# Performance work log

Hardware: AMD Instinct MI355X
Metric: run time of the kernel (lower is better)

The kernel has to match this reference:

```python
import jax, jax.numpy as jnp
import numpy as np

H = 2880      # hidden_size
NH = 64       # num query heads
NKV = 8       # num kv heads
D = 64        # head_dim
G = NH // NKV # GQA group size
W = 128       # sliding window (keys per query, incl. self)
THETA = 150000.0
N = 1024      # tokens


def setup_inputs() -> dict:
    key = jax.random.key(0)
    k0, k1, k2, k3 = jax.random.split(key, 4)
    hidden_states = jax.random.normal(k0, (N, H), jnp.float32)
    Wqkv = jax.random.normal(k1, (H, (NH + 2 * NKV) * D), jnp.float32) * (H ** -0.5)
    Wo = jax.random.normal(k2, (NH * D, H), jnp.float32) * ((NH * D) ** -0.5)
    sinks = jax.random.normal(k3, (NH,), jnp.float32)
    positions = jnp.arange(N, dtype=jnp.int64)
    return {"hidden_states": hidden_states, "Wqkv": Wqkv, "Wo": Wo,
            "sinks": sinks, "positions": positions}


def _rope(x, pos):
    # NeoX-style rotary over full head_dim. x: [n, h, D], pos: [n]
    half = D // 2
    inv_freq = 1.0 / (THETA ** (jnp.arange(half, dtype=jnp.float32) / half))
    ang = pos[:, None].astype(jnp.float32) * inv_freq          # [n, half]
    cos = jnp.cos(ang)[:, None, :]
    sin = jnp.sin(ang)[:, None, :]
    x1, x2 = x[..., :half], x[..., half:]
    return jnp.concatenate([x1 * cos - x2 * sin, x2 * cos + x1 * sin], axis=-1)


def reference(hidden_states, Wqkv, Wo, sinks, positions):
    n = hidden_states.shape[0]
    qkv = hidden_states @ Wqkv
    q, k, v = jnp.split(qkv, [NH * D, NH * D + NKV * D], axis=-1)
    q = _rope(q.reshape(n, NH, D), positions)   # [n, NH, D]
    k = _rope(k.reshape(n, NKV, D), positions)  # [n, NKV, D]
    v = v.reshape(n, NKV, D)

    # Sliding-window key indices: query i attends keys j in [i-W+1, i]
    idx = positions[:, None] - (W - 1) + jnp.arange(W)[None, :]  # [n, W]
    valid = idx >= 0
    idx = jnp.clip(idx, 0, n - 1)
    k_win = k[idx]  # [n, W, NKV, D]
    v_win = v[idx]  # [n, W, NKV, D]

    qg = q.reshape(n, NKV, G, D)
    scores = jnp.einsum('nkgd,nwkd->nkgw', qg, k_win) * (D ** -0.5)
    scores = jnp.where(valid[:, None, None, :], scores, -jnp.inf)

    # Attention sinks: softmax over [scores, sink_logit]; sink gets no value.
    sink = sinks.reshape(NKV, G)                      # [NKV, G]
    m = jnp.maximum(scores.max(-1), sink[None])       # [n, NKV, G]
    p = jnp.exp(scores - m[..., None])                # [n, NKV, G, W]
    denom = p.sum(-1) + jnp.exp(sink[None] - m)       # [n, NKV, G]
    out = jnp.einsum('nkgw,nwkd->nkgd', p, v_win) / denom[..., None]
    return out.reshape(n, NH * D) @ Wo
```

## Files before the change

kernel.cpp:

```cpp
#include <hip/hip_runtime.h>
#include <hip/hip_bf16.h>

#define HDIM   2880
#define NH     64
#define NKV    8
#define DHEAD  64
#define GQ     (NH / NKV)
#define WIN    128
#define NTOK   1024
#define QKV_N  ((NH + 2 * NKV) * DHEAD)
#define QCOLS  (NH * DHEAD)
#define KOFF   QCOLS
#define VOFF   (QCOLS + NKV * DHEAD)

typedef __attribute__((ext_vector_type(8))) short short8;
typedef __attribute__((ext_vector_type(4))) float floatx4;

__device__ unsigned short g_Xb   [(size_t)NTOK  * HDIM];
__device__ unsigned short g_qkvb [(size_t)NTOK  * QKV_N];
__device__ unsigned short g_attn [(size_t)NTOK  * QCOLS];
__device__ unsigned short g_WqkvT[(size_t)QKV_N * HDIM];
__device__ unsigned short g_WoT  [(size_t)HDIM * QCOLS];

__device__ __forceinline__ unsigned short f2b(float f) {
    __hip_bfloat16 h = __float2bfloat16(f);
    return *reinterpret_cast<unsigned short*>(&h);
}

__device__ __forceinline__ void gload_lds16(const unsigned short* g, unsigned short* l) {
    __builtin_amdgcn_global_load_lds(
        (const __attribute__((address_space(1))) unsigned int*)g,
        (__attribute__((address_space(3))) unsigned int*)l, 16, 0, 0);
}

__device__ __forceinline__ void transpose_tile(
        const float* __restrict__ in, unsigned short* __restrict__ out,
        int K, int N, int bk, int bn, int t, unsigned short* T) {
    #pragma unroll
    for (int i = 0; i < 4; ++i) {
        int c = i * 256 + t;
        int r = c >> 4, cc = (c & 15) * 4;
        float4 v = *(const float4*)(in + (size_t)(bk * 64 + r) * N + bn * 64 + cc);
        int col = (((cc >> 2) ^ ((r >> 3) & 7)) << 2);
        T[r * 72 + col + 0] = f2b(v.x);
        T[r * 72 + col + 1] = f2b(v.y);
        T[r * 72 + col + 2] = f2b(v.z);
        T[r * 72 + col + 3] = f2b(v.w);
    }
    __syncthreads();
    #pragma unroll
    for (int i = 0; i < 2; ++i) {
        int c = i * 256 + t;
        int rn = c >> 3, kc = (c & 7) * 8;
        int s = (kc >> 3) & 7;
        int col = ((((rn >> 2) ^ s) << 2) | (rn & 3));
        int4 vv;
        unsigned short* tp = (unsigned short*)&vv;
        #pragma unroll
        for (int j = 0; j < 8; ++j) tp[j] = T[(kc + j) * 72 + col];
        *(int4*)(out + (size_t)(bn * 64 + rn) * K + bk * 64 + kc) = vv;
    }
}

#define NB_WQKV (45 * 80)
#define NB_WO   (64 * 45)
#define NB_CVT  (NTOK * HDIM / 4 / 256)
__global__ __launch_bounds__(256) void prep(
        const float* __restrict__ X, const float* __restrict__ Wqkv,
        const float* __restrict__ Wo, unsigned short* __restrict__ Xb,
        unsigned short* __restrict__ WqkvT, unsigned short* __restrict__ WoT) {
    __shared__ __align__(16) unsigned short T[64 * 72];
    int id = blockIdx.x;
    int t = threadIdx.x;
    if (id < NB_WQKV) {
        transpose_tile(Wqkv, WqkvT, HDIM, QKV_N, id % 45, id / 45, t, T);
    } else if (id < NB_WQKV + NB_WO) {
        int id2 = id - NB_WQKV;
        transpose_tile(Wo, WoT, QCOLS, HDIM, id2 % 64, id2 / 64, t, T);
    } else {
        int gid = (id - NB_WQKV - NB_WO) * 256 + t;
        float4 v = *(const float4*)(X + (size_t)gid * 4);
        ushort4 o;
        o.x = f2b(v.x); o.y = f2b(v.y); o.z = f2b(v.z); o.w = f2b(v.w);
        *(ushort4*)(Xb + (size_t)gid * 4) = o;
    }
}

template<int KLEN, int MODE, int NBN>
__global__ __launch_bounds__(256) void gemm_dir(
        const unsigned short* __restrict__ A, const unsigned short* __restrict__ Bt,
        void* __restrict__ outp) {
    int d0 = blockIdx.x;
    int work = (d0 & 7) * NBN + (d0 >> 3);
    int bm = work & 7, bn = work >> 3;
    int t = threadIdx.x, lane = t & 63, wid = t >> 6;
    int quad = lane >> 4, ml = lane & 15;
    __shared__ __align__(16) unsigned short As[2][128 * 64];
    __shared__ __align__(16) unsigned short Bs[2][64 * 64];
    floatx4 acc[2][4];
    #pragma unroll
    for (int i = 0; i < 2; ++i)
        #pragma unroll
        for (int j = 0; j < 4; ++j) acc[i][j] = (floatx4){0.f, 0.f, 0.f, 0.f};

    int srow = lane >> 3;
    int scol = ((lane & 7) ^ srow) * 8;
    const unsigned short* Ab = A  + (size_t)(bm * 128) * KLEN;
    const unsigned short* Bb = Bt + (size_t)(bn * 64) * KLEN;

    constexpr int NT = KLEN / 64;

    #pragma unroll
    for (int j = 0; j < 4; ++j) {
        int grp = wid * 4 + j;
        int r = grp * 8 + srow;
        gload_lds16(Ab + (size_t)r * KLEN + scol, &As[0][grp * 512]);
    }
    #pragma unroll
    for (int j = 0; j < 2; ++j) {
        int grp = wid * 2 + j;
        int r = grp * 8 + srow;
        gload_lds16(Bb + (size_t)r * KLEN + scol, &Bs[0][grp * 512]);
    }
    __syncthreads();

    for (int ti = 0; ti < NT; ++ti) {
        int cur = ti & 1;
        if (ti + 1 < NT) {
            int k0 = (ti + 1) * 64;
            int nxt = cur ^ 1;
            #pragma unroll
            for (int j = 0; j < 4; ++j) {
                int grp = wid * 4 + j;
                int r = grp * 8 + srow;
                gload_lds16(Ab + (size_t)r * KLEN + k0 + scol, &As[nxt][grp * 512]);
            }
            #pragma unroll
            for (int j = 0; j < 2; ++j) {
                int grp = wid * 2 + j;
                int r = grp * 8 + srow;
                gload_lds16(Bb + (size_t)r * KLEN + k0 + scol, &Bs[nxt][grp * 512]);
            }
        }
        #pragma unroll
        for (int kk = 0; kk < 64; kk += 32) {
            const int ub = kk >> 3;
            int usw = ((ub + quad) ^ (ml & 7)) * 8;
            short8 af[2], bf[4];
            #pragma unroll
            for (int mt = 0; mt < 2; ++mt)
                af[mt] = *(const short8*)&As[cur][(wid * 32 + mt * 16 + ml) * 64 + usw];
            #pragma unroll
            for (int nt = 0; nt < 4; ++nt)
                bf[nt] = *(const short8*)&Bs[cur][(nt * 16 + ml) * 64 + usw];
            #pragma unroll
            for (int mt = 0; mt < 2; ++mt)
                #pragma unroll
                for (int nt = 0; nt < 4; ++nt)
                    acc[mt][nt] = __builtin_amdgcn_mfma_f32_16x16x32_bf16(af[mt], bf[nt], acc[mt][nt], 0, 0, 0);
        }
        __syncthreads();
    }

    if constexpr (MODE == 0) {
        unsigned short* qp = (unsigned short*)outp;
        int cb = bn * 64;
        if (bn < NH + NKV) {
            float inv0 = expf(-(float)ml * 0.3724497053f);
            float inv1 = expf(-(float)(16 + ml) * 0.3724497053f);
            #pragma unroll
            for (int mt = 0; mt < 2; ++mt) {
                #pragma unroll
                for (int r = 0; r < 4; ++r) {
                    int n = bm * 128 + wid * 32 + mt * 16 + quad * 4 + r;
                    unsigned short* op = qp + (size_t)n * QKV_N + cb;
                    float s0, c0, s1, c1;
                    sincosf((float)n * inv0, &s0, &c0);
                    sincosf((float)n * inv1, &s1, &c1);
                    float x1a = acc[mt][0][r], x2a = acc[mt][2][r];
                    float x1b = acc[mt][1][r], x2b = acc[mt][3][r];
                    op[ml]           = f2b(x1a * c0 - x2a * s0);
                    op[ml + 32]      = f2b(x2a * c0 + x1a * s0);
                    op[16 + ml]      = f2b(x1b * c1 - x2b * s1);
                    op[16 + ml + 32] = f2b(x2b * c1 + x1b * s1);
                }
            }
        } else {
            #pragma unroll
            for (int mt = 0; mt < 2; ++mt)
                #pragma unroll
                for (int r = 0; r < 4; ++r) {
                    int n = bm * 128 + wid * 32 + mt * 16 + quad * 4 + r;
                    unsigned short* op = qp + (size_t)n * QKV_N + cb;
                    #pragma unroll
                    for (int nt = 0; nt < 4; ++nt)
                        op[nt * 16 + ml] = f2b(acc[mt][nt][r]);
                }
        }
    } else {
        float* op0 = (float*)outp;
        #pragma unroll
        for (int mt = 0; mt < 2; ++mt)
            #pragma unroll
            for (int r = 0; r < 4; ++r) {
                int n = bm * 128 + wid * 32 + mt * 16 + quad * 4 + r;
                float* op = op0 + (size_t)n * HDIM + bn * 64;
                #pragma unroll
                for (int nt = 0; nt < 4; ++nt)
                    op[nt * 16 + ml] = acc[mt][nt][r];
            }
    }
}

#define TQ     16
#define VT_LD  200
#define PS_LD  168

__global__ __launch_bounds__(256) void attn_mfma(
        const unsigned short* __restrict__ qkvb,
        const float* __restrict__ sinks,
        unsigned short* __restrict__ aout) {
    int d0 = blockIdx.x;
    int work = (d0 & 7) * 64 + (d0 >> 3);
    int t0 = (work & 63) * TQ, kh = work >> 6;
    int t = threadIdx.x, lane = t & 63, wid = t >> 6;
    int quad = lane >> 4, ml = lane & 15;
    int wavebase = wid * 32;

    __shared__ __align__(16) unsigned short Vt[DHEAD * VT_LD];
    __shared__ __align__(16) unsigned short Ps[4 * 16 * PS_LD];
    unsigned short* Psw = &Ps[wid * 16 * PS_LD];

    #pragma unroll
    for (int i = 0; i < 5; ++i) {
        int c = i * 256 + t;
        int w = c >> 3, d8 = (c & 7) * 8;
        int r = t0 - 127 + w;
        r = min(max(r, 0), NTOK - 1);
        int4 vv = *(const int4*)(qkvb + (size_t)r * QKV_N + VOFF + kh * DHEAD + d8);
        const unsigned short* vp = (const unsigned short*)&vv;
        int wc = ((((w >> 3) ^ (d8 >> 3)) << 3) | (w & 7));
        #pragma unroll
        for (int j = 0; j < 8; ++j) Vt[(d8 + j) * VT_LD + wc] = vp[j];
    }
    __syncthreads();

    short8 qf[2][2];
    #pragma unroll
    for (int mt = 0; mt < 2; ++mt) {
        int m = wavebase + mt * 16 + ml;
        int tl = m & 15, g = m >> 4;
        const unsigned short* qp = qkvb + (size_t)(t0 + tl) * QKV_N + (kh * GQ + g) * DHEAD;
        #pragma unroll
        for (int kk = 0; kk < 2; ++kk)
            qf[mt][kk] = *(const short8*)(qp + kk * 32 + quad * 8);
    }

    const unsigned short* Kbase = qkvb + KOFF + kh * DHEAD;
    floatx4 S[2][10];
    #pragma unroll
    for (int mt = 0; mt < 2; ++mt)
        #pragma unroll
        for (int nt = 0; nt < 10; ++nt) S[mt][nt] = (floatx4){0.f, 0.f, 0.f, 0.f};
    #pragma unroll
    for (int kk = 0; kk < 2; ++kk) {
        #pragma unroll
        for (int nt = 0; nt < 10; ++nt) {
            int r = t0 - 127 + nt * 16 + ml;
            r = min(max(r, 0), NTOK - 1);
            short8 kb = *(const short8*)(Kbase + (size_t)r * QKV_N + kk * 32 + quad * 8);
            #pragma unroll
            for (int mt = 0; mt < 2; ++mt)
                S[mt][nt] = __builtin_amdgcn_mfma_f32_16x16x32_bf16(qf[mt][kk], kb, S[mt][nt], 0, 0, 0);
        }
    }

    int wmin0 = 127 - t0;
    #pragma unroll
    for (int mt = 0; mt < 2; ++mt) {
        #pragma unroll
        for (int r = 0; r < 4; ++r) {
            int tl = (wavebase + mt * 16 + quad * 4 + r) & 15;
            int wlo = tl > wmin0 ? tl : wmin0;
            int whi = tl + 127;
            #pragma unroll
            for (int nt = 0; nt < 10; ++nt) {
                int w = nt * 16 + ml;
                float s = S[mt][nt][r] * 0.125f;
                S[mt][nt][r] = (w >= wlo && w <= whi) ? s : -INFINITY;
            }
        }
    }

    #pragma unroll
    for (int mt = 0; mt < 2; ++mt) {
        int g = (wavebase + mt * 16) >> 4;
        float sk = sinks[kh * GQ + g];
        #pragma unroll
        for (int r = 0; r < 4; ++r) {
            float rm = -INFINITY;
            #pragma unroll
            for (int nt = 0; nt < 10; ++nt) rm = fmaxf(rm, S[mt][nt][r]);
            #pragma unroll
            for (int off = 1; off < 16; off <<= 1) rm = fmaxf(rm, __shfl_xor(rm, off));
            rm = fmaxf(rm, sk);
            float sum = 0.f;
            #pragma unroll
            for (int nt = 0; nt < 10; ++nt) {
                float p = __expf(S[mt][nt][r] - rm);
                S[mt][nt][r] = p;
                sum += p;
            }
            #pragma unroll
            for (int off = 1; off < 16; off <<= 1) sum += __shfl_xor(sum, off);
            float inv = 1.f / (sum + __expf(sk - rm));
            #pragma unroll
            for (int nt = 0; nt < 10; ++nt) S[mt][nt][r] *= inv;
        }
    }

    #pragma unroll
    for (int mt = 0; mt < 2; ++mt) {
        #pragma unroll
        for (int r = 0; r < 4; ++r) {
            int lr = quad * 4 + r;
            #pragma unroll
            for (int nt = 0; nt < 10; ++nt)
                Psw[lr * PS_LD + nt * 16 + ml] = f2b(S[mt][nt][r]);
        }
        floatx4 O[4];
        #pragma unroll
        for (int j = 0; j < 4; ++j) O[j] = (floatx4){0.f, 0.f, 0.f, 0.f};
        #pragma unroll
        for (int ks = 0; ks < 5; ++ks) {
            short8 pf = *(const short8*)&Psw[ml * PS_LD + ks * 32 + quad * 8];
            #pragma unroll
            for (int nt = 0; nt < 4; ++nt) {
                int d = nt * 16 + ml;
                int u = ((ks * 4 + quad) ^ ((d >> 3) & 7)) << 3;
                short8 vf = *(const short8*)&Vt[d * VT_LD + u];
                O[nt] = __builtin_amdgcn_mfma_f32_16x16x32_bf16(pf, vf, O[nt], 0, 0, 0);
            }
        }
        #pragma unroll
        for (int r = 0; r < 4; ++r) {
            int mm = wavebase + mt * 16 + quad * 4 + r;
            int tl = mm & 15, g = mm >> 4;
            unsigned short* op = aout + (size_t)(t0 + tl) * QCOLS + (kh * GQ + g) * DHEAD;
            #pragma unroll
            for (int nt = 0; nt < 4; ++nt)
                op[nt * 16 + ml] = f2b(O[nt][r]);
        }
    }
}

extern "C" void kernel_launch(void* const* d_in, const int* in_sizes, int n_in,
                              void* d_out, int out_size, void* d_ws, size_t ws_size,
                              hipStream_t stream) {
    const float* X     = (const float*)d_in[0];
    const float* Wqkv  = (const float*)d_in[1];
    const float* Wo    = (const float*)d_in[2];
    const float* sinks = (const float*)d_in[3];
    float* out = (float*)d_out;

    unsigned short *Xb, *qkvb, *attn, *WqkvT, *WoT;
    hipGetSymbolAddress((void**)&Xb,    HIP_SYMBOL(g_Xb));
    hipGetSymbolAddress((void**)&qkvb,  HIP_SYMBOL(g_qkvb));
    hipGetSymbolAddress((void**)&attn,  HIP_SYMBOL(g_attn));
    hipGetSymbolAddress((void**)&WqkvT, HIP_SYMBOL(g_WqkvT));
    hipGetSymbolAddress((void**)&WoT,   HIP_SYMBOL(g_WoT));

    prep<<<NB_WQKV + NB_WO + NB_CVT, 256, 0, stream>>>(X, Wqkv, Wo, Xb, WqkvT, WoT);

    gemm_dir<HDIM, 0, QKV_N / 64><<<8 * (QKV_N / 64), 256, 0, stream>>>(Xb, WqkvT, qkvb);

    attn_mfma<<<512, 256, 0, stream>>>(qkvb, sinks, attn);

    gemm_dir<QCOLS, 1, HDIM / 64><<<8 * (HDIM / 64), 256, 0, stream>>>(attn, WoT, out);
}
```

Baseline: 310.9 us.

## Move Wo transpose into attention launch and raise MFMA wave priority

The Wo transpose/bf16 conversion blocks move out of the prep kernel and are appended as extra blocks to the attention kernel. This lets that memory-bound work overlap with the attention computation, which alone fills only 512 blocks. The attention LDS is merged into one shared buffer so the transpose blocks can reuse it. s_setprio is raised around the MFMA loops to favour compute waves over the co-resident transpose blocks. The risk is that the extra blocks contend for bandwidth or lengthen the attention launch's tail.

```diff
diff --git a/kernel.cpp b/kernel.cpp
--- a/kernel.cpp
+++ b/kernel.cpp
@@ -65,20 +65,16 @@
 #define NB_WQKV (45 * 80)
 #define NB_WO   (64 * 45)
 #define NB_CVT  (NTOK * HDIM / 4 / 256)
-__global__ __launch_bounds__(256) void prep(
+__global__ __launch_bounds__(256) void prep1(
         const float* __restrict__ X, const float* __restrict__ Wqkv,
-        const float* __restrict__ Wo, unsigned short* __restrict__ Xb,
-        unsigned short* __restrict__ WqkvT, unsigned short* __restrict__ WoT) {
+        unsigned short* __restrict__ Xb, unsigned short* __restrict__ WqkvT) {
     __shared__ __align__(16) unsigned short T[64 * 72];
     int id = blockIdx.x;
     int t = threadIdx.x;
     if (id < NB_WQKV) {
         transpose_tile(Wqkv, WqkvT, HDIM, QKV_N, id % 45, id / 45, t, T);
-    } else if (id < NB_WQKV + NB_WO) {
-        int id2 = id - NB_WQKV;
-        transpose_tile(Wo, WoT, QCOLS, HDIM, id2 % 64, id2 / 64, t, T);
     } else {
-        int gid = (id - NB_WQKV - NB_WO) * 256 + t;
+        int gid = (id - NB_WQKV) * 256 + t;
         float4 v = *(const float4*)(X + (size_t)gid * 4);
         ushort4 o;
         o.x = f2b(v.x); o.y = f2b(v.y); o.z = f2b(v.z); o.w = f2b(v.w);
@@ -215,20 +211,32 @@
 #define TQ     16
 #define VT_LD  200
 #define PS_LD  168
-
-__global__ __launch_bounds__(256) void attn_mfma(
+#define ATTN_NB 512
+
+__global__ __launch_bounds__(256) void attn_fused(
         const unsigned short* __restrict__ qkvb,
         const float* __restrict__ sinks,
-        unsigned short* __restrict__ aout) {
+        unsigned short* __restrict__ aout,
+        const float* __restrict__ Wo,
+        unsigned short* __restrict__ WoT) {
+    __shared__ __align__(16) unsigned short LDSb[DHEAD * VT_LD + 4 * 16 * PS_LD];
     int d0 = blockIdx.x;
+    int t = threadIdx.x;
+
+    if (d0 >= ATTN_NB) {
+        int id2 = d0 - ATTN_NB;
+        transpose_tile(Wo, WoT, QCOLS, HDIM, id2 % 64, id2 / 64, t, LDSb);
+        return;
+    }
+
     int work = (d0 & 7) * 64 + (d0 >> 3);
     int t0 = (work & 63) * TQ, kh = work >> 6;
-    int t = threadIdx.x, lane = t & 63, wid = t >> 6;
+    int lane = t & 63, wid = t >> 6;
     int quad = lane >> 4, ml = lane & 15;
     int wavebase = wid * 32;
 
-    __shared__ __align__(16) unsigned short Vt[DHEAD * VT_LD];
-    __shared__ __align__(16) unsigned short Ps[4 * 16 * PS_LD];
+    unsigned short* Vt = LDSb;
+    unsigned short* Ps = LDSb + DHEAD * VT_LD;
     unsigned short* Psw = &Ps[wid * 16 * PS_LD];
 
     #pragma unroll
@@ -262,6 +270,7 @@
     for (int mt = 0; mt < 2; ++mt)
         #pragma unroll
         for (int nt = 0; nt < 10; ++nt) S[mt][nt] = (floatx4){0.f, 0.f, 0.f, 0.f};
+    __builtin_amdgcn_s_setprio(1);
     #pragma unroll
     for (int kk = 0; kk < 2; ++kk) {
         #pragma unroll
@@ -274,6 +283,7 @@
                 S[mt][nt] = __builtin_amdgcn_mfma_f32_16x16x32_bf16(qf[mt][kk], kb, S[mt][nt], 0, 0, 0);
         }
     }
+    __builtin_amdgcn_s_setprio(0);
 
     int wmin0 = 127 - t0;
     #pragma unroll
@@ -331,6 +341,7 @@
         floatx4 O[4];
         #pragma unroll
         for (int j = 0; j < 4; ++j) O[j] = (floatx4){0.f, 0.f, 0.f, 0.f};
+        __builtin_amdgcn_s_setprio(1);
         #pragma unroll
         for (int ks = 0; ks < 5; ++ks) {
             short8 pf = *(const short8*)&Psw[ml * PS_LD + ks * 32 + quad * 8];
@@ -342,6 +353,7 @@
                 O[nt] = __builtin_amdgcn_mfma_f32_16x16x32_bf16(pf, vf, O[nt], 0, 0, 0);
             }
         }
+        __builtin_amdgcn_s_setprio(0);
         #pragma unroll
         for (int r = 0; r < 4; ++r) {
             int mm = wavebase + mt * 16 + quad * 4 + r;
@@ -370,11 +382,11 @@
     hipGetSymbolAddress((void**)&WqkvT, HIP_SYMBOL(g_WqkvT));
     hipGetSymbolAddress((void**)&WoT,   HIP_SYMBOL(g_WoT));
 
-    prep<<<NB_WQKV + NB_WO + NB_CVT, 256, 0, stream>>>(X, Wqkv, Wo, Xb, WqkvT, WoT);
+    prep1<<<NB_WQKV + NB_CVT, 256, 0, stream>>>(X, Wqkv, Xb, WqkvT);
 
     gemm_dir<HDIM, 0, QKV_N / 64><<<8 * (QKV_N / 64), 256, 0, stream>>>(Xb, WqkvT, qkvb);
 
-    attn_mfma<<<512, 256, 0, stream>>>(qkvb, sinks, attn);
+    attn_fused<<<ATTN_NB + NB_WO, 256, 0, stream>>>(qkvb, sinks, attn, Wo, WoT);
 
     gemm_dir<QCOLS, 1, HDIM / 64><<<8 * (HDIM / 64), 256, 0, stream>>>(attn, WoT, out);
 }
```

New measurement: 307.8 us. Within noise of the previous version (-1.0%).
